# Kernel tuning notes

Hardware: AMD Instinct MI355X
Metric: run time of the kernel (lower is better)

## Reference

```python
import jax, jax.numpy as jnp
import numpy as np
import math

B, H, W, C = 2, 112, 112, 128
NUM_HEADS = 4
RADIUS = 2


def setup_inputs() -> dict:
    key = jax.random.key(0)
    k0, k1, k2 = jax.random.split(key, 3)
    x = jax.random.normal(k0, (B, H, W, C), dtype=jnp.float32)
    # Linear weights stored as [in, out] (transpose of torch's [out, in])
    w_qkv = jax.random.normal(k1, (C, 3 * C), dtype=jnp.float32) * (1.0 / math.sqrt(C))
    b_qkv = jnp.zeros((3 * C,), dtype=jnp.float32)
    w_out = jax.random.normal(k2, (C, C), dtype=jnp.float32) * (1.0 / math.sqrt(C))
    b_out = jnp.zeros((C,), dtype=jnp.float32)
    return {"x": x, "w_qkv": w_qkv, "b_qkv": b_qkv, "w_out": w_out, "b_out": b_out}


def _local_window_attn(x, w_qkv, b_qkv, w_out, b_out):
    b, h, w, c = x.shape
    hd = c // NUM_HEADS
    ws1 = 2 * RADIUS + 1          # window side
    ws = ws1 * ws1                # window size
    scale = 1.0 / math.sqrt(hd)

    # The torch module projects patches (copies of pixels) with a per-pixel
    # Linear; projection commutes with reflect-pad/gather, so project first.
    qkv = x @ w_qkv + b_qkv                       # [B,H,W,3C]
    q, kf, vf = jnp.split(qkv, 3, axis=-1)        # each [B,H,W,C]

    pad = ((0, 0), (RADIUS, RADIUS), (RADIUS, RADIUS), (0, 0))
    kp = jnp.pad(kf, pad, mode="reflect")
    vp = jnp.pad(vf, pad, mode="reflect")

    def patches(t):  # [B,H+2r,W+2r,C] -> [B,H,W,ws,C]
        return jnp.stack(
            [t[:, dy:dy + h, dx:dx + w, :] for dy in range(ws1) for dx in range(ws1)],
            axis=3,
        )

    kpat = patches(kp).reshape(b, h, w, ws, NUM_HEADS, hd)
    vpat = patches(vp).reshape(b, h, w, ws, NUM_HEADS, hd)
    qh = q.reshape(b, h, w, NUM_HEADS, hd)

    scores = jnp.einsum("bxynd,bxywnd->bxynw", qh, kpat) * scale  # [B,H,W,nh,ws]
    attn = jax.nn.softmax(scores, axis=-1)
    out = jnp.einsum("bxynw,bxywnd->bxynd", attn, vpat).reshape(b, h, w, c)
    return out @ w_out + b_out


def reference(x, w_qkv, b_qkv, w_out, b_out):
    return _local_window_attn(x, w_qkv, b_qkv, w_out, b_out)
```

## Files before the change

### kernel.cpp

```cpp
#include <hip/hip_runtime.h>
#include <hip/hip_bf16.h>
#include <math.h>

#define BATCH 2
#define HH 112
#define WW 112
#define CC 128
#define NHEADS 4
#define HD 32
#define RAD 2
#define WS1 5
#define WSZ 25
#define M_TOT (BATCH * HH * WW)

template <int BM, int BN, int BK, int TM, int TN, int K>
__global__ __launch_bounds__(256)
void gemm_bias_kernel(const float* __restrict__ A, const float* __restrict__ Bw,
                      const float* __restrict__ bias, float* __restrict__ Cout,
                      int M, int N) {
    __shared__ float As[BK][BM + 4];
    __shared__ float Bs[BK][BN];

    constexpr int TCOLS = BN / TN;
    static_assert((BM / TM) * (BN / TN) == 256, "256 threads");

    const int tid = threadIdx.x;
    const int tn = tid % TCOLS;
    const int tm = tid / TCOLS;
    const int m0 = blockIdx.x * BM;
    const int n0 = blockIdx.y * BN;

    constexpr int A_F4 = BM * BK / 4;
    constexpr int B_F4 = BK * BN / 4;

    const int ar0 = tid / (BK / 4);
    const int ac4 = tid % (BK / 4);
    const int br0 = tid / (BN / 4);
    const int bc4 = tid % (BN / 4);

    float acc[TM][TN] = {};

#pragma unroll 1
    for (int k0 = 0; k0 < K; k0 += BK) {
#pragma unroll
        for (int l = 0; l < A_F4 / 256; ++l) {
            int r = ar0 + l * (256 / (BK / 4));
            float4 v = *reinterpret_cast<const float4*>(
                &A[(size_t)(m0 + r) * K + k0 + ac4 * 4]);
            As[ac4 * 4 + 0][r] = v.x;
            As[ac4 * 4 + 1][r] = v.y;
            As[ac4 * 4 + 2][r] = v.z;
            As[ac4 * 4 + 3][r] = v.w;
        }
#pragma unroll
        for (int l = 0; l < B_F4 / 256; ++l) {
            int r = br0 + l * (256 / (BN / 4));
            *reinterpret_cast<float4*>(&Bs[r][bc4 * 4]) =
                *reinterpret_cast<const float4*>(
                    &Bw[(size_t)(k0 + r) * N + n0 + bc4 * 4]);
        }
        __syncthreads();

#pragma unroll
        for (int k = 0; k < BK; ++k) {
            float a[TM], b[TN];
#pragma unroll
            for (int i = 0; i < TM; i += 4) {
                float4 v = *reinterpret_cast<const float4*>(&As[k][tm * TM + i]);
                a[i] = v.x; a[i + 1] = v.y; a[i + 2] = v.z; a[i + 3] = v.w;
            }
#pragma unroll
            for (int j = 0; j < TN; j += 4) {
                float4 v = *reinterpret_cast<const float4*>(&Bs[k][tn * TN + j]);
                b[j] = v.x; b[j + 1] = v.y; b[j + 2] = v.z; b[j + 3] = v.w;
            }
#pragma unroll
            for (int i = 0; i < TM; ++i)
#pragma unroll
                for (int j = 0; j < TN; ++j) acc[i][j] += a[i] * b[j];
        }
        __syncthreads();
    }

#pragma unroll
    for (int i = 0; i < TM; ++i) {
        int m = m0 + tm * TM + i;
#pragma unroll
        for (int j = 0; j < TN; j += 4) {
            int n = n0 + tn * TN + j;
            float4 o;
            o.x = acc[i][j + 0] + bias[n + 0];
            o.y = acc[i][j + 1] + bias[n + 1];
            o.z = acc[i][j + 2] + bias[n + 2];
            o.w = acc[i][j + 3] + bias[n + 3];
            *reinterpret_cast<float4*>(&Cout[(size_t)m * N + n]) = o;
        }
    }
}

__global__ __launch_bounds__(256)
void attn_kernel(const float* __restrict__ qkv, float* __restrict__ attn_out) {
    const int tid = threadIdx.x;
    const int sub = tid & 15;
    const int pix = blockIdx.x * 16 + (tid >> 4);
    const int c0 = sub * 8;

    const int bw = pix / (HH * WW);
    const int rem = pix - bw * (HH * WW);
    const int y = rem / WW;
    const int x = rem - y * WW;
    const float scale = 0.1767766952966369f;

    const float4 q0 = *reinterpret_cast<const float4*>(&qkv[(size_t)pix * 384 + c0]);
    const float4 q1 = *reinterpret_cast<const float4*>(&qkv[(size_t)pix * 384 + c0 + 4]);

    float s[WSZ];
    int np[WSZ];

#pragma unroll
    for (int dy = 0; dy < WS1; ++dy) {
        int yy = y + dy - RAD;
        yy = yy < 0 ? -yy : (yy >= HH ? 2 * (HH - 1) - yy : yy);
#pragma unroll
        for (int dx = 0; dx < WS1; ++dx) {
            int xx = x + dx - RAD;
            xx = xx < 0 ? -xx : (xx >= WW ? 2 * (WW - 1) - xx : xx);
            const int wi = dy * WS1 + dx;
            const int n = (bw * HH + yy) * WW + xx;
            np[wi] = n;
            const float4 k0 =
                *reinterpret_cast<const float4*>(&qkv[(size_t)n * 384 + 128 + c0]);
            const float4 k1 =
                *reinterpret_cast<const float4*>(&qkv[(size_t)n * 384 + 128 + c0 + 4]);
            float partial = q0.x * k0.x + q0.y * k0.y + q0.z * k0.z + q0.w * k0.w +
                            q1.x * k1.x + q1.y * k1.y + q1.z * k1.z + q1.w * k1.w;
            partial += __shfl_xor(partial, 1);
            partial += __shfl_xor(partial, 2);
            s[wi] = partial * scale;
        }
    }

    float mx = s[0];
#pragma unroll
    for (int i = 1; i < WSZ; ++i) mx = fmaxf(mx, s[i]);
    float sum = 0.f;
#pragma unroll
    for (int i = 0; i < WSZ; ++i) {
        s[i] = __expf(s[i] - mx);
        sum += s[i];
    }
    const float inv = 1.0f / sum;

    float4 o0 = make_float4(0.f, 0.f, 0.f, 0.f);
    float4 o1 = make_float4(0.f, 0.f, 0.f, 0.f);
#pragma unroll
    for (int i = 0; i < WSZ; ++i) {
        const float4 v0 =
            *reinterpret_cast<const float4*>(&qkv[(size_t)np[i] * 384 + 256 + c0]);
        const float4 v1 =
            *reinterpret_cast<const float4*>(&qkv[(size_t)np[i] * 384 + 256 + c0 + 4]);
        const float p = s[i] * inv;
        o0.x += p * v0.x; o0.y += p * v0.y; o0.z += p * v0.z; o0.w += p * v0.w;
        o1.x += p * v1.x; o1.y += p * v1.y; o1.z += p * v1.z; o1.w += p * v1.w;
    }

    *reinterpret_cast<float4*>(&attn_out[(size_t)pix * 128 + c0]) = o0;
    *reinterpret_cast<float4*>(&attn_out[(size_t)pix * 128 + c0 + 4]) = o1;
}

extern "C" void kernel_launch(void* const* d_in, const int* in_sizes, int n_in,
                              void* d_out, int out_size, void* d_ws, size_t ws_size,
                              hipStream_t stream) {
    const float* x = (const float*)d_in[0];
    const float* w_qkv = (const float*)d_in[1];
    const float* b_qkv = (const float*)d_in[2];
    const float* w_out = (const float*)d_in[3];
    const float* b_out = (const float*)d_in[4];
    float* out = (float*)d_out;

    float* qkv = (float*)d_ws;
    float* attn_out = qkv + (size_t)M_TOT * 3 * CC;

    {
        dim3 grid(M_TOT / 128, (3 * CC) / 128);
        gemm_bias_kernel<128, 128, 32, 8, 8, CC><<<grid, 256, 0, stream>>>(
            x, w_qkv, b_qkv, qkv, M_TOT, 3 * CC);
    }

    {
        dim3 grid(M_TOT / 16);
        attn_kernel<<<grid, 256, 0, stream>>>(qkv, attn_out);
    }

    {
        dim3 grid(M_TOT / 128, CC / 64);
        gemm_bias_kernel<128, 64, 32, 8, 4, CC><<<grid, 256, 0, stream>>>(
            attn_out, w_out, b_out, out, M_TOT, CC);
    }
}
```

Baseline: 161.7 us.

## Replace FP32 SIMT GEMMs with split-bf16 MFMA GEMMs for both projections

Both linear projections now run on matrix cores. Inputs and weights are split into bf16 high and low parts, and three MFMA products (hi*hi, hi*lo, lo*hi) approximate fp32 accuracy. Weights are pre-split and transposed by a small kernel on every call, while activations are split on the fly while being staged into LDS. The intent is to cut the FP32 FMA cost of the GEMMs, at the price of extra conversion work, two extra launches and scalar (non-vectorised) output stores.

```diff
diff --git a/kernel.cpp b/kernel.cpp
--- a/kernel.cpp
+++ b/kernel.cpp
@@ -7,93 +7,115 @@
 #define WW 112
 #define CC 128
 #define NHEADS 4
-#define HD 32
 #define RAD 2
 #define WS1 5
 #define WSZ 25
 #define M_TOT (BATCH * HH * WW)
 
-template <int BM, int BN, int BK, int TM, int TN, int K>
+typedef __attribute__((ext_vector_type(8))) short bf16x8;
+typedef __attribute__((ext_vector_type(4))) float f32x4;
+
+__device__ __forceinline__ ushort bf16_rne(float x) {
+    unsigned u = __float_as_uint(x);
+    unsigned r = u + 0x7FFFu + ((u >> 16) & 1u);
+    return (ushort)(r >> 16);
+}
+__device__ __forceinline__ float bf16_to_f(ushort h) {
+    return __uint_as_float(((unsigned)h) << 16);
+}
+
 __global__ __launch_bounds__(256)
-void gemm_bias_kernel(const float* __restrict__ A, const float* __restrict__ Bw,
-                      const float* __restrict__ bias, float* __restrict__ Cout,
-                      int M, int N) {
-    __shared__ float As[BK][BM + 4];
-    __shared__ float Bs[BK][BN];
-
-    constexpr int TCOLS = BN / TN;
-    static_assert((BM / TM) * (BN / TN) == 256, "256 threads");
+void wsplit_kernel(const float* __restrict__ W, ushort* __restrict__ Wt_hi,
+                   ushort* __restrict__ Wt_lo, int N) {
+    int idx = blockIdx.x * 256 + threadIdx.x;
+    int k = idx / N;
+    int n = idx - k * N;
+    float x = W[idx];
+    ushort h = bf16_rne(x);
+    float rem = x - bf16_to_f(h);
+    ushort l = bf16_rne(rem);
+    Wt_hi[n * CC + k] = h;
+    Wt_lo[n * CC + k] = l;
+}
+
+#define LDKP 40
+__global__ __launch_bounds__(256, 3)
+void gemm_mfma_kernel(const float* __restrict__ A, const ushort* __restrict__ Wt_hi,
+                      const ushort* __restrict__ Wt_lo, const float* __restrict__ bias,
+                      float* __restrict__ Cout, int M, int N) {
+    __shared__ ushort Ah[128][LDKP], Al[128][LDKP];
+    __shared__ ushort Bh[64][LDKP], Bl[64][LDKP];
 
     const int tid = threadIdx.x;
-    const int tn = tid % TCOLS;
-    const int tm = tid / TCOLS;
-    const int m0 = blockIdx.x * BM;
-    const int n0 = blockIdx.y * BN;
-
-    constexpr int A_F4 = BM * BK / 4;
-    constexpr int B_F4 = BK * BN / 4;
-
-    const int ar0 = tid / (BK / 4);
-    const int ac4 = tid % (BK / 4);
-    const int br0 = tid / (BN / 4);
-    const int bc4 = tid % (BN / 4);
-
-    float acc[TM][TN] = {};
+    const int wave = tid >> 6;
+    const int lane = tid & 63;
+    const int fr = lane & 15;
+    const int fq = lane >> 4;
+    const int m0 = blockIdx.x * 128;
+    const int n0 = blockIdx.y * 64;
+
+    f32x4 acc[2][4] = {};
 
 #pragma unroll 1
-    for (int k0 = 0; k0 < K; k0 += BK) {
-#pragma unroll
-        for (int l = 0; l < A_F4 / 256; ++l) {
-            int r = ar0 + l * (256 / (BK / 4));
+    for (int kt = 0; kt < 4; ++kt) {
+        const int kb = kt * 32;
+#pragma unroll
+        for (int i = 0; i < 4; ++i) {
+            int f4 = tid + i * 256;
+            int r = f4 >> 3, c4 = f4 & 7;
             float4 v = *reinterpret_cast<const float4*>(
-                &A[(size_t)(m0 + r) * K + k0 + ac4 * 4]);
-            As[ac4 * 4 + 0][r] = v.x;
-            As[ac4 * 4 + 1][r] = v.y;
-            As[ac4 * 4 + 2][r] = v.z;
-            As[ac4 * 4 + 3][r] = v.w;
-        }
-#pragma unroll
-        for (int l = 0; l < B_F4 / 256; ++l) {
-            int r = br0 + l * (256 / (BN / 4));
-            *reinterpret_cast<float4*>(&Bs[r][bc4 * 4]) =
-                *reinterpret_cast<const float4*>(
-                    &Bw[(size_t)(k0 + r) * N + n0 + bc4 * 4]);
+                &A[(size_t)(m0 + r) * CC + kb + c4 * 4]);
+            ushort h0 = bf16_rne(v.x), h1 = bf16_rne(v.y);
+            ushort h2 = bf16_rne(v.z), h3 = bf16_rne(v.w);
+            ushort l0 = bf16_rne(v.x - bf16_to_f(h0));
+            ushort l1 = bf16_rne(v.y - bf16_to_f(h1));
+            ushort l2 = bf16_rne(v.z - bf16_to_f(h2));
+            ushort l3 = bf16_rne(v.w - bf16_to_f(h3));
+            *reinterpret_cast<ushort4*>(&Ah[r][c4 * 4]) = make_ushort4(h0, h1, h2, h3);
+            *reinterpret_cast<ushort4*>(&Al[r][c4 * 4]) = make_ushort4(l0, l1, l2, l3);
+        }
+        {
+            int r = tid >> 2, c8 = tid & 3;
+            *reinterpret_cast<uint4*>(&Bh[r][c8 * 8]) = *reinterpret_cast<const uint4*>(
+                &Wt_hi[(size_t)(n0 + r) * CC + kb + c8 * 8]);
+            *reinterpret_cast<uint4*>(&Bl[r][c8 * 8]) = *reinterpret_cast<const uint4*>(
+                &Wt_lo[(size_t)(n0 + r) * CC + kb + c8 * 8]);
         }
         __syncthreads();
 
-#pragma unroll
-        for (int k = 0; k < BK; ++k) {
-            float a[TM], b[TN];
-#pragma unroll
-            for (int i = 0; i < TM; i += 4) {
-                float4 v = *reinterpret_cast<const float4*>(&As[k][tm * TM + i]);
-                a[i] = v.x; a[i + 1] = v.y; a[i + 2] = v.z; a[i + 3] = v.w;
+        const int kk = fq * 8;
+        bf16x8 bh[4], bl[4];
+#pragma unroll
+        for (int nt = 0; nt < 4; ++nt) {
+            bh[nt] = *reinterpret_cast<const bf16x8*>(&Bh[nt * 16 + fr][kk]);
+            bl[nt] = *reinterpret_cast<const bf16x8*>(&Bl[nt * 16 + fr][kk]);
+        }
+#pragma unroll
+        for (int mt = 0; mt < 2; ++mt) {
+            const int row = wave * 32 + mt * 16 + fr;
+            bf16x8 ah = *reinterpret_cast<const bf16x8*>(&Ah[row][kk]);
+            bf16x8 al = *reinterpret_cast<const bf16x8*>(&Al[row][kk]);
+#pragma unroll
+            for (int nt = 0; nt < 4; ++nt) {
+                acc[mt][nt] = __builtin_amdgcn_mfma_f32_16x16x32_bf16(ah, bh[nt], acc[mt][nt], 0, 0, 0);
+                acc[mt][nt] = __builtin_amdgcn_mfma_f32_16x16x32_bf16(ah, bl[nt], acc[mt][nt], 0, 0, 0);
+                acc[mt][nt] = __builtin_amdgcn_mfma_f32_16x16x32_bf16(al, bh[nt], acc[mt][nt], 0, 0, 0);
             }
-#pragma unroll
-            for (int j = 0; j < TN; j += 4) {
-                float4 v = *reinterpret_cast<const float4*>(&Bs[k][tn * TN + j]);
-                b[j] = v.x; b[j + 1] = v.y; b[j + 2] = v.z; b[j + 3] = v.w;
+        }
+        __syncthreads();
+    }
+
+#pragma unroll
+    for (int mt = 0; mt < 2; ++mt) {
+#pragma unroll
+        for (int nt = 0; nt < 4; ++nt) {
+            const int n = n0 + nt * 16 + fr;
+            const float bv = bias[n];
+#pragma unroll
+            for (int r = 0; r < 4; ++r) {
+                const int m = m0 + wave * 32 + mt * 16 + fq * 4 + r;
+                Cout[(size_t)m * N + n] = acc[mt][nt][r] + bv;
             }
-#pragma unroll
-            for (int i = 0; i < TM; ++i)
-#pragma unroll
-                for (int j = 0; j < TN; ++j) acc[i][j] += a[i] * b[j];
-        }
-        __syncthreads();
-    }
-
-#pragma unroll
-    for (int i = 0; i < TM; ++i) {
-        int m = m0 + tm * TM + i;
-#pragma unroll
-        for (int j = 0; j < TN; j += 4) {
-            int n = n0 + tn * TN + j;
-            float4 o;
-            o.x = acc[i][j + 0] + bias[n + 0];
-            o.y = acc[i][j + 1] + bias[n + 1];
-            o.z = acc[i][j + 2] + bias[n + 2];
-            o.w = acc[i][j + 3] + bias[n + 3];
-            *reinterpret_cast<float4*>(&Cout[(size_t)m * N + n]) = o;
         }
     }
 }
@@ -180,21 +202,19 @@
 
     float* qkv = (float*)d_ws;
     float* attn_out = qkv + (size_t)M_TOT * 3 * CC;
-
-    {
-        dim3 grid(M_TOT / 128, (3 * CC) / 128);
-        gemm_bias_kernel<128, 128, 32, 8, 8, CC><<<grid, 256, 0, stream>>>(
-            x, w_qkv, b_qkv, qkv, M_TOT, 3 * CC);
-    }
-
-    {
-        dim3 grid(M_TOT / 16);
-        attn_kernel<<<grid, 256, 0, stream>>>(qkv, attn_out);
-    }
-
-    {
-        dim3 grid(M_TOT / 128, CC / 64);
-        gemm_bias_kernel<128, 64, 32, 8, 4, CC><<<grid, 256, 0, stream>>>(
-            attn_out, w_out, b_out, out, M_TOT, CC);
-    }
-}
+    ushort* wq_hi = (ushort*)(attn_out + (size_t)M_TOT * CC);
+    ushort* wq_lo = wq_hi + 384 * CC;
+    ushort* wo_hi = wq_lo + 384 * CC;
+    ushort* wo_lo = wo_hi + CC * CC;
+
+    wsplit_kernel<<<(CC * 384) / 256, 256, 0, stream>>>(w_qkv, wq_hi, wq_lo, 384);
+    wsplit_kernel<<<(CC * CC) / 256, 256, 0, stream>>>(w_out, wo_hi, wo_lo, CC);
+
+    gemm_mfma_kernel<<<dim3(M_TOT / 128, 384 / 64), 256, 0, stream>>>(
+        x, wq_hi, wq_lo, b_qkv, qkv, M_TOT, 384);
+
+    attn_kernel<<<M_TOT / 16, 256, 0, stream>>>(qkv, attn_out);
+
+    gemm_mfma_kernel<<<dim3(M_TOT / 128, CC / 64), 256, 0, stream>>>(
+        attn_out, wo_hi, wo_lo, b_out, out, M_TOT, CC);
+}
```

Result: faster. 136.2 us (-15.8%).
